# Optimization experiments

Hardware: AMD Instinct MI355X
Metric: run time of the kernel (lower is better)

Reference implementation:

```python
import jax, jax.numpy as jnp
import numpy as np

B, C, H, W = 2, 64, 256, 256
DW = 128          # c * DW_Expand
FFN = 128         # c * FFN_Expand
GRID = 8          # wH = wW modulation grid


def setup_inputs() -> dict:
    key = jax.random.key(0)
    ks = jax.random.split(key, 16)
    rn = lambda k, s, sc=1.0: jax.random.normal(k, s, jnp.float32) * sc
    return {
        "x": rn(ks[0], (B, C, H, W)),
        "w1": rn(ks[1], (DW, C), (2.0 / C) ** 0.5),
        "b1": jnp.zeros((DW,), jnp.float32),
        "w2": rn(ks[2], (DW, 3, 3), (2.0 / 9.0) ** 0.5),
        "b2": jnp.zeros((DW,), jnp.float32),
        "w3": rn(ks[3], (C, DW // 2), (2.0 / (DW // 2)) ** 0.5),
        "b3": jnp.zeros((C,), jnp.float32),
        "sca_w": rn(ks[4], (DW // 2, DW // 2), (1.0 / (DW // 2)) ** 0.5),
        "sca_b": jnp.zeros((DW // 2,), jnp.float32),
        "w4": rn(ks[5], (FFN, C), (2.0 / C) ** 0.5),
        "b4": jnp.zeros((FFN,), jnp.float32),
        "w5": rn(ks[6], (C, FFN // 2), (2.0 / (FFN // 2)) ** 0.5),
        "b5": jnp.zeros((C,), jnp.float32),
        "n1_w": jnp.ones((C,), jnp.float32),
        "n1_b": jnp.zeros((C,), jnp.float32),
        "n2_w": jnp.ones((C,), jnp.float32),
        "n2_b": jnp.zeros((C,), jnp.float32),
        "beta": rn(ks[7], (C,), 0.1),
        "gamma": rn(ks[8], (C,), 0.1),
        "mod1": rn(ks[9], (B, DW, C, GRID, GRID)),
        "mod2": rn(ks[10], (B, DW, GRID, GRID)),
        "mod3": rn(ks[11], (B, C, DW // 2, GRID, GRID)),
        "mod4": rn(ks[12], (B, FFN, C, GRID, GRID)),
        "mod5": rn(ks[13], (B, C, FFN // 2, GRID, GRID)),
    }


def layernorm2d(x, w, b, eps=1e-6):
    # channel-wise LayerNorm per pixel (NAFNet LayerNorm2d)
    mu = jnp.mean(x, axis=1, keepdims=True)
    var = jnp.mean((x - mu) ** 2, axis=1, keepdims=True)
    return (x - mu) / jnp.sqrt(var + eps) * w[None, :, None, None] + b[None, :, None, None]


def conv1x1_modulated(x, wb, bb, mod):
    # wb: [Co,Ci], mod: [B,Co,Ci,wH,wW]; per-patch 1x1 conv with normalized dynamic weights
    w = wb[None, :, :, None, None] * mod                      # [B,Co,Ci,wH,wW]
    w = w / jnp.sqrt(jnp.sum(w * w, axis=2, keepdims=True))   # normalize over Ci (kh*kw==1)
    b_, ci, h, wd = x.shape
    wh, ww = mod.shape[-2:]
    ph, pw = h // wh, wd // ww
    xp = x.reshape(b_, ci, wh, ph, ww, pw)                    # split into patches
    y = jnp.einsum('bocuv,bcupvq->boupvq', w, xp)             # per-patch matmul
    return y.reshape(b_, wb.shape[0], h, wd) + bb[None, :, None, None]


def conv3x3_dw_modulated(x, wb, bb, mod):
    # wb: [C,3,3], mod: [B,C,wH,wW]; per-patch depthwise 3x3, padding 1 across whole image
    w = wb[None, :, :, :, None, None] * mod[:, :, None, None, :, :]  # [B,C,3,3,wH,wW]
    w = w / jnp.sqrt(jnp.sum(w * w, axis=(2, 3), keepdims=True))     # normalize over (ci=1, kh*kw)
    b_, c, h, wd = x.shape
    wh, ww = mod.shape[-2:]
    ph, pw = h // wh, wd // ww
    xpad = jnp.pad(x, ((0, 0), (0, 0), (1, 1), (1, 1)))
    out = jnp.zeros_like(x)
    for dh in range(3):
        for dw_ in range(3):
            xs = xpad[:, :, dh:dh + h, dw_:dw_ + wd].reshape(b_, c, wh, ph, ww, pw)
            wk = w[:, :, dh, dw_, :, :]                        # [B,C,wH,wW]
            out = out + (wk[:, :, :, None, :, None] * xs).reshape(b_, c, h, wd)
    return out + bb[None, :, None, None]


def simple_gate(x):
    a, g = jnp.split(x, 2, axis=1)
    return a * g


def reference(x, w1, b1, w2, b2, w3, b3, sca_w, sca_b, w4, b4, w5, b5,
              n1_w, n1_b, n2_w, n2_b, beta, gamma, mod1, mod2, mod3, mod4, mod5):
    y = layernorm2d(x, n1_w, n1_b)
    y = conv1x1_modulated(y, w1, b1, mod1)
    y = conv3x3_dw_modulated(y, w2, b2, mod2)
    y = simple_gate(y)
    s = jnp.mean(y, axis=(2, 3), keepdims=True)               # SCA: global pool + 1x1
    s = jnp.einsum('oc,bcij->boij', sca_w, s) + sca_b[None, :, None, None]
    y = y * s
    y = conv1x1_modulated(y, w3, b3, mod3)
    y1 = x + y * beta[None, :, None, None]
    z = conv1x1_modulated(layernorm2d(y1, n2_w, n2_b), w4, b4, mod4)
    z = simple_gate(z)
    z = conv1x1_modulated(z, w5, b5, mod5)
    return y1 + z * gamma[None, :, None, None]
```

## Files before the change

### kernel.cpp

```cpp
#include <hip/hip_runtime.h>
#include <hip/hip_bf16.h>


typedef __bf16 bf16x8 __attribute__((ext_vector_type(8)));
typedef float f32x4 __attribute__((ext_vector_type(4)));
typedef unsigned short u16x8 __attribute__((ext_vector_type(8)));

__device__ __forceinline__ float b2f(unsigned short u) {
    union { unsigned int i; float f; } x; x.i = ((unsigned int)u) << 16; return x.f;
}
__device__ __forceinline__ unsigned short f2b(float f) {
    union { float f; unsigned int i; } x; x.f = f;
    unsigned int i = x.i;
    return (unsigned short)((i + 0x7FFFu + ((i >> 16) & 1u)) >> 16);
}
__device__ __forceinline__ unsigned int pk2(float a, float b) {
    __hip_bfloat162 h = __float22bfloat162_rn(float2{a, b});
    union { __hip_bfloat162 h; unsigned int u; } cv; cv.h = h; return cv.u;
}

__global__ __launch_bounds__(256) void prep_k(
    const float* __restrict__ w1, const float* __restrict__ mod1,
    const float* __restrict__ w3, const float* __restrict__ mod3,
    const float* __restrict__ beta,
    const float* __restrict__ w4, const float* __restrict__ mod4,
    const float* __restrict__ w5, const float* __restrict__ mod5,
    const float* __restrict__ gam,
    unsigned short* __restrict__ pw1, unsigned short* __restrict__ pw3,
    unsigned short* __restrict__ pw4, unsigned short* __restrict__ pw5,
    float* __restrict__ s0)
{
    const int tid = threadIdx.x;
    int blk = blockIdx.x;
    if (blk == 0 && tid < 128) s0[tid] = 0.f;
    const float* w; const float* mod; const float* rows = nullptr;
    unsigned short* out; int NOUT; int rem;
    if (blk < 256)      { w = w1; mod = mod1; out = pw1; NOUT = 128; rem = blk; }
    else if (blk < 384) { w = w3; mod = mod3; out = pw3; NOUT = 64;  rem = blk - 256; rows = beta; }
    else if (blk < 640) { w = w4; mod = mod4; out = pw4; NOUT = 128; rem = blk - 384; }
    else                { w = w5; mod = mod5; out = pw5; NOUT = 64;  rem = blk - 640; rows = gam; }
    const int b = rem / NOUT, o = rem % NOUT;

    __shared__ float mlds[64 * 68];
    __shared__ float wlsh[64];
    __shared__ float red[4 * 64];
    __shared__ float rs[64];

    const float* mbase = mod + ((size_t)(b * NOUT + o) * 64) * 64;
#pragma unroll
    for (int k = 0; k < 4; ++k) {
        int l = tid + k * 256;
        float4 vv = ((const float4*)mbase)[l];
        int c = l >> 4, q = l & 15;
        *(float4*)&mlds[c * 68 + q * 4] = vv;
    }
    if (tid < 64) wlsh[tid] = w[o * 64 + tid];
    __syncthreads();

    {
        int uv = tid & 63, part = tid >> 6;
        float ss = 0.f;
#pragma unroll
        for (int j = 0; j < 16; ++j) {
            int c = part * 16 + j;
            float t = wlsh[c] * mlds[c * 68 + uv];
            ss += t * t;
        }
        red[part * 64 + uv] = ss;
    }
    __syncthreads();
    if (tid < 64) {
        float tot = red[tid] + red[64 + tid] + red[128 + tid] + red[192 + tid];
        rs[tid] = rsqrtf(fmaxf(tot, 1e-30f)) * (rows ? rows[o] : 1.f);
    }
    __syncthreads();

    {
        int uvw = tid >> 2, cp = tid & 3;
        float r = rs[uvw];
        size_t obase = ((size_t)(b * 64 + uvw) * NOUT + o) * 64;
#pragma unroll
        for (int g = 0; g < 2; ++g) {
            u16x8 pk;
#pragma unroll
            for (int e = 0; e < 8; ++e) {
                int c = cp * 16 + g * 8 + e;
                pk[e] = f2b(wlsh[c] * mlds[c * 68 + uvw] * r);
            }
            *(u16x8*)&out[obase + cp * 16 + g * 8] = pk;
        }
    }
}

__global__ __launch_bounds__(256, 2) void head_k(
    const float* __restrict__ x, unsigned short* __restrict__ t1,
    const unsigned short* __restrict__ pw1, const float* __restrict__ b1,
    const float* __restrict__ n1w, const float* __restrict__ n1b, int bbase)
{
    const int tid   = threadIdx.x;
    const int uv    = blockIdx.x;
    const int chunk = blockIdx.y;
    const int z     = blockIdx.z;
    const int bfull = z + bbase;
    const int u = uv >> 3, v = uv & 7;
    const int h_base = u * 32 + chunk * 4;
    const int w_base = v * 32;

    __shared__ __align__(16) unsigned short stage[128 * 72];

    const int wave = tid >> 6;
    const int lane = tid & 63;
    const int q = lane >> 4;
    const int r = lane & 15;
    const int nfi[2] = {2 * wave, 2 * wave + 1};

    const unsigned short* pwt = pw1 + ((size_t)(bfull * 64 + uv) * 128) * 64;
    bf16x8 bfr[2][2];
#pragma unroll
    for (int f = 0; f < 2; ++f)
#pragma unroll
        for (int ks = 0; ks < 2; ++ks)
            bfr[f][ks] = *(const bf16x8*)&pwt[(16 * nfi[f] + r) * 64 + ks * 32 + q * 8];
    float bsc[2] = {b1[16 * nfi[0] + r], b1[16 * nfi[1] + r]};

    const int cg = tid & 7;
    const int qd = tid >> 3;
    const int c0 = cg * 8;
    const int pixg = (h_base + (qd >> 3)) * 256 + w_base + (qd & 7) * 4;
    float v2[8][4];
#pragma unroll
    for (int k = 0; k < 8; ++k) {
        float4 t = *(const float4*)&x[((z * 64 + c0 + k) << 16) + pixg];
        v2[k][0] = t.x; v2[k][1] = t.y; v2[k][2] = t.z; v2[k][3] = t.w;
    }
    float lw[8], lb[8];
    *(float4*)&lw[0] = *(const float4*)&n1w[c0];
    *(float4*)&lw[4] = *(const float4*)&n1w[c0 + 4];
    *(float4*)&lb[0] = *(const float4*)&n1b[c0];
    *(float4*)&lb[4] = *(const float4*)&n1b[c0 + 4];
#pragma unroll
    for (int e = 0; e < 4; ++e) {
        float s1 = 0.f, s2 = 0.f;
#pragma unroll
        for (int k = 0; k < 8; ++k) { s1 += v2[k][e]; s2 += v2[k][e] * v2[k][e]; }
#pragma unroll
        for (int m = 1; m < 8; m <<= 1) { s1 += __shfl_xor(s1, m); s2 += __shfl_xor(s2, m); }
        float mu = s1 * (1.f / 64.f);
        float var = s2 * (1.f / 64.f) - mu * mu;
        float rstd = rsqrtf(fmaxf(var, 0.f) + 1e-6f);
        float o8[8];
#pragma unroll
        for (int k = 0; k < 8; ++k) o8[k] = (v2[k][e] - mu) * rstd * lw[k] + lb[k];
        uint4 pk;
        pk.x = pk2(o8[0], o8[1]); pk.y = pk2(o8[2], o8[3]);
        pk.z = pk2(o8[4], o8[5]); pk.w = pk2(o8[6], o8[7]);
        *(uint4*)&stage[(qd * 4 + e) * 72 + c0] = pk;
    }

    __syncthreads();

    f32x4 acc[8][2];
#pragma unroll
    for (int mi = 0; mi < 8; ++mi) { acc[mi][0] = (f32x4){0,0,0,0}; acc[mi][1] = (f32x4){0,0,0,0}; }
#pragma unroll
    for (int mi = 0; mi < 8; ++mi) {
        bf16x8 a0 = *(const bf16x8*)&stage[(16 * mi + r) * 72 + q * 8];
        bf16x8 a1 = *(const bf16x8*)&stage[(16 * mi + r) * 72 + 32 + q * 8];
#pragma unroll
        for (int f = 0; f < 2; ++f) {
            acc[mi][f] = __builtin_amdgcn_mfma_f32_16x16x32_bf16(a0, bfr[f][0], acc[mi][f], 0, 0, 0);
            acc[mi][f] = __builtin_amdgcn_mfma_f32_16x16x32_bf16(a1, bfr[f][1], acc[mi][f], 0, 0, 0);
        }
    }

#pragma unroll
    for (int mi = 0; mi < 8; ++mi) {
        int lp0 = 16 * mi + 4 * q;
        int pix = (h_base + (lp0 >> 5)) * 256 + w_base + (lp0 & 31);
#pragma unroll
        for (int f = 0; f < 2; ++f) {
            int o = 16 * nfi[f] + r;
            float bs = bsc[f];
            *(uint2*)&t1[((z * 128 + o) << 16) + pix] =
                make_uint2(pk2(acc[mi][f][0] + bs, acc[mi][f][1] + bs),
                           pk2(acc[mi][f][2] + bs, acc[mi][f][3] + bs));
        }
    }
}

__global__ __launch_bounds__(256, 2) void tail_k(
    const unsigned short* __restrict__ t3, const float* __restrict__ x,
    float* __restrict__ outp,
    const unsigned short* __restrict__ pw3, const float* __restrict__ b3,
    const float* __restrict__ beta,
    const unsigned short* __restrict__ pw4, const float* __restrict__ b4,
    const float* __restrict__ n2w, const float* __restrict__ n2b,
    const unsigned short* __restrict__ pw5, const float* __restrict__ b5,
    const float* __restrict__ gam,
    const float* __restrict__ scaw, const float* __restrict__ scab,
    const float* __restrict__ s0, int bbase)
{
    const int tid   = threadIdx.x;
    const int uv    = blockIdx.x;
    const int chunk = blockIdx.y;
    const int z     = blockIdx.z;
    const int bfull = z + bbase;
    const int u = uv >> 3, v = uv & 7;
    const int h_base = u * 32 + chunk * 4;
    const int w_base = v * 32;

    __shared__ __align__(16) unsigned short stage[128 * 72];
    __shared__ float sfin_l[64];

    const int wave = tid >> 6;
    const int lane = tid & 63;
    const int q = lane >> 4;
    const int r = lane & 15;
    const int oo = 16 * wave + r;

    if (tid < 64) {
        const float* srow = scaw + tid * 64;
        const float* s0b  = s0 + bfull * 64;
        float acc = 0.f;
#pragma unroll
        for (int c4 = 0; c4 < 16; ++c4) {
            float4 wv = *(const float4*)&srow[c4 * 4];
            float4 s4 = *(const float4*)&s0b[c4 * 4];
            acc += wv.x * s4.x + wv.y * s4.y + wv.z * s4.z + wv.w * s4.w;
        }
        sfin_l[tid] = acc * (1.f / 65536.f) + scab[tid];
    }

    const unsigned short* p3 = pw3 + (size_t)(bfull * 64 + uv) * 64 * 64;
    const unsigned short* p4 = pw4 + (size_t)(bfull * 64 + uv) * 128 * 64;
    const unsigned short* p5 = pw5 + (size_t)(bfull * 64 + uv) * 64 * 64;
    bf16x8 w3f[2], w5f[2], w4f[2][2];
    const int nfi4[2] = {wave, wave + 4};
#pragma unroll
    for (int ks = 0; ks < 2; ++ks) {
        w3f[ks] = *(const bf16x8*)&p3[(oo) * 64 + ks * 32 + q * 8];
        w5f[ks] = *(const bf16x8*)&p5[(oo) * 64 + ks * 32 + q * 8];
#pragma unroll
        for (int f = 0; f < 2; ++f)
            w4f[f][ks] = *(const bf16x8*)&p4[(16 * nfi4[f] + r) * 64 + ks * 32 + q * 8];
    }
    const float sb3 = b3[oo] * beta[oo];
    const float ba4 = b4[oo], bg4 = b4[oo + 64];
    const float sb5 = b5[oo] * gam[oo];

    __syncthreads();

    const int cg = tid & 7;
    const int qd = tid >> 3;
    const int c0 = cg * 8;
    const int pixg = (h_base + (qd >> 3)) * 256 + w_base + (qd & 7) * 4;
    {
        float sv[8];
        *(float4*)&sv[0] = *(const float4*)&sfin_l[c0];
        *(float4*)&sv[4] = *(const float4*)&sfin_l[c0 + 4];
        float v2[8][4];
#pragma unroll
        for (int k = 0; k < 8; ++k) {
            ushort4 t = *(const ushort4*)&t3[((z * 64 + c0 + k) << 16) + pixg];
            v2[k][0] = b2f(t.x) * sv[k]; v2[k][1] = b2f(t.y) * sv[k];
            v2[k][2] = b2f(t.z) * sv[k]; v2[k][3] = b2f(t.w) * sv[k];
        }
#pragma unroll
        for (int e = 0; e < 4; ++e) {
            uint4 pk;
            pk.x = pk2(v2[0][e], v2[1][e]); pk.y = pk2(v2[2][e], v2[3][e]);
            pk.z = pk2(v2[4][e], v2[5][e]); pk.w = pk2(v2[6][e], v2[7][e]);
            *(uint4*)&stage[(qd * 4 + e) * 72 + c0] = pk;
        }
    }
    __syncthreads();

    f32x4 acc3[8];
#pragma unroll
    for (int mi = 0; mi < 8; ++mi) acc3[mi] = (f32x4){0, 0, 0, 0};
#pragma unroll
    for (int mi = 0; mi < 8; ++mi) {
        bf16x8 a0 = *(const bf16x8*)&stage[(16 * mi + r) * 72 + q * 8];
        bf16x8 a1 = *(const bf16x8*)&stage[(16 * mi + r) * 72 + 32 + q * 8];
        acc3[mi] = __builtin_amdgcn_mfma_f32_16x16x32_bf16(a0, w3f[0], acc3[mi], 0, 0, 0);
        acc3[mi] = __builtin_amdgcn_mfma_f32_16x16x32_bf16(a1, w3f[1], acc3[mi], 0, 0, 0);
    }
    __syncthreads();

    float y1v[8][4];
#pragma unroll
    for (int mi = 0; mi < 8; ++mi) {
        int lp0 = 16 * mi + 4 * q;
        int pix = (h_base + (lp0 >> 5)) * 256 + w_base + (lp0 & 31);
        float4 xr = *(const float4*)&x[((z * 64 + oo) << 16) + pix];
        y1v[mi][0] = acc3[mi][0] + sb3 + xr.x;
        y1v[mi][1] = acc3[mi][1] + sb3 + xr.y;
        y1v[mi][2] = acc3[mi][2] + sb3 + xr.z;
        y1v[mi][3] = acc3[mi][3] + sb3 + xr.w;
    }
#pragma unroll
    for (int mi = 0; mi < 8; ++mi)
#pragma unroll
        for (int e = 0; e < 4; ++e)
            stage[(16 * mi + 4 * q + e) * 72 + oo] = f2b(y1v[mi][e]);
    __syncthreads();

    {
        float lw[8], lb[8];
        *(float4*)&lw[0] = *(const float4*)&n2w[c0];
        *(float4*)&lw[4] = *(const float4*)&n2w[c0 + 4];
        *(float4*)&lb[0] = *(const float4*)&n2b[c0];
        *(float4*)&lb[4] = *(const float4*)&n2b[c0 + 4];
#pragma unroll
        for (int e = 0; e < 4; ++e) {
            int px = qd * 4 + e;
            uint4 raw = *(const uint4*)&stage[px * 72 + c0];
            unsigned short* rp = (unsigned short*)&raw;
            float vv[8];
            float s1 = 0.f, s2 = 0.f;
#pragma unroll
            for (int k = 0; k < 8; ++k) { vv[k] = b2f(rp[k]); s1 += vv[k]; s2 += vv[k] * vv[k]; }
#pragma unroll
            for (int m = 1; m < 8; m <<= 1) { s1 += __shfl_xor(s1, m); s2 += __shfl_xor(s2, m); }
            float mu = s1 * (1.f / 64.f);
            float var = s2 * (1.f / 64.f) - mu * mu;
            float rstd = rsqrtf(fmaxf(var, 0.f) + 1e-6f);
            float o8[8];
#pragma unroll
            for (int k = 0; k < 8; ++k) o8[k] = (vv[k] - mu) * rstd * lw[k] + lb[k];
            uint4 pk;
            pk.x = pk2(o8[0], o8[1]); pk.y = pk2(o8[2], o8[3]);
            pk.z = pk2(o8[4], o8[5]); pk.w = pk2(o8[6], o8[7]);
            *(uint4*)&stage[px * 72 + c0] = pk;
        }
    }
    __syncthreads();

    f32x4 acc4[8][2];
#pragma unroll
    for (int mi = 0; mi < 8; ++mi) { acc4[mi][0] = (f32x4){0,0,0,0}; acc4[mi][1] = (f32x4){0,0,0,0}; }
#pragma unroll
    for (int mi = 0; mi < 8; ++mi) {
        bf16x8 a0 = *(const bf16x8*)&stage[(16 * mi + r) * 72 + q * 8];
        bf16x8 a1 = *(const bf16x8*)&stage[(16 * mi + r) * 72 + 32 + q * 8];
#pragma unroll
        for (int f = 0; f < 2; ++f) {
            acc4[mi][f] = __builtin_amdgcn_mfma_f32_16x16x32_bf16(a0, w4f[f][0], acc4[mi][f], 0, 0, 0);
            acc4[mi][f] = __builtin_amdgcn_mfma_f32_16x16x32_bf16(a1, w4f[f][1], acc4[mi][f], 0, 0, 0);
        }
    }
    __syncthreads();
#pragma unroll
    for (int mi = 0; mi < 8; ++mi)
#pragma unroll
        for (int e = 0; e < 4; ++e) {
            float zv = (acc4[mi][0][e] + ba4) * (acc4[mi][1][e] + bg4);
            stage[(16 * mi + 4 * q + e) * 72 + oo] = f2b(zv);
        }
    __syncthreads();

    f32x4 acc5[8];
#pragma unroll
    for (int mi = 0; mi < 8; ++mi) acc5[mi] = (f32x4){0, 0, 0, 0};
#pragma unroll
    for (int mi = 0; mi < 8; ++mi) {
        bf16x8 a0 = *(const bf16x8*)&stage[(16 * mi + r) * 72 + q * 8];
        bf16x8 a1 = *(const bf16x8*)&stage[(16 * mi + r) * 72 + 32 + q * 8];
        acc5[mi] = __builtin_amdgcn_mfma_f32_16x16x32_bf16(a0, w5f[0], acc5[mi], 0, 0, 0);
        acc5[mi] = __builtin_amdgcn_mfma_f32_16x16x32_bf16(a1, w5f[1], acc5[mi], 0, 0, 0);
    }
#pragma unroll
    for (int mi = 0; mi < 8; ++mi) {
        int lp0 = 16 * mi + 4 * q;
        int pix = (h_base + (lp0 >> 5)) * 256 + w_base + (lp0 & 31);
        *(float4*)&outp[((z * 64 + oo) << 16) + pix] =
            make_float4(y1v[mi][0] + acc5[mi][0] + sb5,
                        y1v[mi][1] + acc5[mi][1] + sb5,
                        y1v[mi][2] + acc5[mi][2] + sb5,
                        y1v[mi][3] + acc5[mi][3] + sb5);
    }
}

__global__ __launch_bounds__(256, 4) void dw_k(
    const unsigned short* __restrict__ t1,
    unsigned short* __restrict__ t3,
    const float* __restrict__ w2,
    const float* __restrict__ b2,
    const float* __restrict__ mod2,
    float* __restrict__ s0,
    int bbase)
{
    const int tid  = threadIdx.x;
    const int oc   = blockIdx.x;
    const int band = blockIdx.y;
    const int z    = blockIdx.z;
    const int bfull = z + bbase;
    const int u = band >> 2;

    __shared__ float wl[2][8][9];
    __shared__ float wred[4];

    if (tid < 16) {
        int halfc = tid >> 3, vv = tid & 7;
        const float* wrow = w2 + (oc + halfc * 64) * 9;
        float wloc[9], ssum = 0.f;
#pragma unroll
        for (int k = 0; k < 9; ++k) { wloc[k] = wrow[k]; ssum += wloc[k] * wloc[k]; }
        float m = mod2[(bfull * 128 + oc + halfc * 64) * 64 + u * 8 + vv];
        float rn = m * rsqrtf(fmaxf(m * m * ssum, 1e-30f));
#pragma unroll
        for (int k = 0; k < 9; ++k) wl[halfc][vv][k] = wloc[k] * rn;
    }
    __syncthreads();

    const int strip = tid & 31;
    const int row   = band * 8 + (tid >> 5);
    const int v     = strip >> 2;

    float wa[9], wg[9];
#pragma unroll
    for (int k = 0; k < 9; ++k) { wa[k] = wl[0][v][k]; wg[k] = wl[1][v][k]; }
    const float ba = b2[oc], bg = b2[oc + 64];

    const unsigned short* pa = t1 + (((size_t)z * 128 + oc) << 16);
    const unsigned short* pg = pa + ((size_t)64 << 16);

    float fa[3][8], fg[3][8], la[3], ra[3], lg[3], rg[3];
#pragma unroll
    for (int dr = 0; dr < 3; ++dr) {
        int rr = row - 1 + dr;
        if (rr >= 0 && rr < 256) {
            u16x8 va = *(const u16x8*)&pa[rr * 256 + strip * 8];
            u16x8 vg = *(const u16x8*)&pg[rr * 256 + strip * 8];
#pragma unroll
            for (int e = 0; e < 8; ++e) { fa[dr][e] = b2f(va[e]); fg[dr][e] = b2f(vg[e]); }
        } else {
#pragma unroll
            for (int e = 0; e < 8; ++e) { fa[dr][e] = 0.f; fg[dr][e] = 0.f; }
        }
        float t;
        t = __shfl_up(fa[dr][7], 1);   la[dr] = (strip == 0)  ? 0.f : t;
        t = __shfl_up(fg[dr][7], 1);   lg[dr] = (strip == 0)  ? 0.f : t;
        t = __shfl_down(fa[dr][0], 1); ra[dr] = (strip == 31) ? 0.f : t;
        t = __shfl_down(fg[dr][0], 1); rg[dr] = (strip == 31) ? 0.f : t;
    }

    float psum = 0.f;
    u16x8 pk;
#pragma unroll
    for (int j = 0; j < 8; ++j) {
        float a = 0.f, g = 0.f;
#pragma unroll
        for (int dr = 0; dr < 3; ++dr) {
            float m1a = (j == 0) ? la[dr] : fa[dr][j - 1];
            float p1a = (j == 7) ? ra[dr] : fa[dr][j + 1];
            float m1g = (j == 0) ? lg[dr] : fg[dr][j - 1];
            float p1g = (j == 7) ? rg[dr] : fg[dr][j + 1];
            a += wa[dr * 3] * m1a + wa[dr * 3 + 1] * fa[dr][j] + wa[dr * 3 + 2] * p1a;
            g += wg[dr * 3] * m1g + wg[dr * 3 + 1] * fg[dr][j] + wg[dr * 3 + 2] * p1g;
        }
        float val = (a + ba) * (g + bg);
        psum += val;
        pk[j] = f2b(val);
    }
    *(u16x8*)&t3[(((size_t)z * 64 + oc) << 16) + row * 256 + strip * 8] = pk;

    for (int off = 32; off > 0; off >>= 1) psum += __shfl_down(psum, off, 64);
    if ((tid & 63) == 0) wred[tid >> 6] = psum;
    __syncthreads();
    if (tid == 0)
        atomicAdd(&s0[bfull * 64 + oc], wred[0] + wred[1] + wred[2] + wred[3]);
}

extern "C" void kernel_launch(void* const* d_in, const int* in_sizes, int n_in,
                              void* d_out, int out_size, void* d_ws, size_t ws_size,
                              hipStream_t stream) {
    (void)in_sizes; (void)n_in; (void)out_size;
    const float* x    = (const float*)d_in[0];
    const float* w1   = (const float*)d_in[1];
    const float* b1   = (const float*)d_in[2];
    const float* w2   = (const float*)d_in[3];
    const float* b2   = (const float*)d_in[4];
    const float* w3   = (const float*)d_in[5];
    const float* b3   = (const float*)d_in[6];
    const float* scaw = (const float*)d_in[7];
    const float* scab = (const float*)d_in[8];
    const float* w4   = (const float*)d_in[9];
    const float* b4   = (const float*)d_in[10];
    const float* w5   = (const float*)d_in[11];
    const float* b5   = (const float*)d_in[12];
    const float* n1w  = (const float*)d_in[13];
    const float* n1b  = (const float*)d_in[14];
    const float* n2w  = (const float*)d_in[15];
    const float* n2b  = (const float*)d_in[16];
    const float* beta = (const float*)d_in[17];
    const float* gam  = (const float*)d_in[18];
    const float* mod1 = (const float*)d_in[19];
    const float* mod2 = (const float*)d_in[20];
    const float* mod3 = (const float*)d_in[21];
    const float* mod4 = (const float*)d_in[22];
    const float* mod5 = (const float*)d_in[23];

    char* ws = (char*)d_ws;
    float* outf = (float*)d_out;

    const size_t IMGel = (size_t)64 * 65536;
    const size_t T1B   = (size_t)128 * 65536 * 2;
    const size_t T3B   = (size_t)64 * 65536 * 2;
    const size_t PW1B = 2097152, PW3B = 1048576, PW4B = 2097152, PW5B = 1048576;
    const size_t TBLB = PW1B + PW3B + PW4B + PW5B;

    const size_t needA = 2 * (T1B + T3B) + 4096 + TBLB;
    const bool planA = ws_size >= needA;
    const size_t NBT = planA ? 2 : 1;

    unsigned short* t1 = (unsigned short*)ws;
    unsigned short* t3 = (unsigned short*)(ws + NBT * T1B);
    char* statb = ws + NBT * (T1B + T3B);
    float* s0   = (float*)statb;
    unsigned short* pw1 = (unsigned short*)(statb + 4096);
    unsigned short* pw3 = (unsigned short*)(statb + 4096 + PW1B);
    unsigned short* pw4 = (unsigned short*)(statb + 4096 + PW1B + PW3B);
    unsigned short* pw5 = (unsigned short*)(statb + 4096 + PW1B + PW3B + PW4B);

    dim3 blk(256);

    prep_k<<<768, blk, 0, stream>>>(w1, mod1, w3, mod3, beta, w4, mod4,
                                    w5, mod5, gam, pw1, pw3, pw4, pw5, s0);

    if (planA) {
        dim3 gconv(64, 8, 2), gdw(64, 32, 2);
        head_k<<<gconv, blk, 0, stream>>>(x, t1, pw1, b1, n1w, n1b, 0);
        dw_k<<<gdw, blk, 0, stream>>>(t1, t3, w2, b2, mod2, s0, 0);
        tail_k<<<gconv, blk, 0, stream>>>(t3, x, outf, pw3, b3, beta,
                                          pw4, b4, n2w, n2b, pw5, b5, gam,
                                          scaw, scab, s0, 0);
    } else {
        for (int bb = 0; bb < 2; ++bb) {
            const float* x_b   = x    + (size_t)bb * IMGel;
            float*       out_b = outf + (size_t)bb * IMGel;
            dim3 gconv(64, 8, 1), gdw(64, 32, 1);
            head_k<<<gconv, blk, 0, stream>>>(x_b, t1, pw1, b1, n1w, n1b, bb);
            dw_k<<<gdw, blk, 0, stream>>>(t1, t3, w2, b2, mod2, s0, bb);
            tail_k<<<gconv, blk, 0, stream>>>(t3, x_b, out_b, pw3, b3, beta,
                                              pw4, b4, n2w, n2b, pw5, b5, gam,
                                              scaw, scab, s0, bb);
        }
    }
}
```

Before: 202.3 us.

## Raise occupancy bounds, prefetch residual, nontemporal output stores, per-thread dw weights

Raises the launch-bounds occupancy hints for head_k to 4 and tail_k to 3 blocks per CU. tail_k now loads the residual x values at kernel entry so their latency overlaps the earlier phases, and it writes the output with nontemporal stores. dw_k drops the shared-memory weight setup and its barrier, and each thread instead computes its own normalized 3x3 weights. The higher occupancy targets can force register spills, and the early x prefetch keeps 32 extra live registers across the kernel.

```diff
diff --git a/kernel.cpp b/kernel.cpp
--- a/kernel.cpp
+++ b/kernel.cpp
@@ -92,7 +92,7 @@
     }
 }
 
-__global__ __launch_bounds__(256, 2) void head_k(
+__global__ __launch_bounds__(256, 4) void head_k(
     const float* __restrict__ x, unsigned short* __restrict__ t1,
     const unsigned short* __restrict__ pw1, const float* __restrict__ b1,
     const float* __restrict__ n1w, const float* __restrict__ n1b, int bbase)
@@ -188,7 +188,7 @@
     }
 }
 
-__global__ __launch_bounds__(256, 2) void tail_k(
+__global__ __launch_bounds__(256, 3) void tail_k(
     const unsigned short* __restrict__ t3, const float* __restrict__ x,
     float* __restrict__ outp,
     const unsigned short* __restrict__ pw3, const float* __restrict__ b3,
@@ -218,6 +218,14 @@
     const int r = lane & 15;
     const int oo = 16 * wave + r;
 
+    float4 xr8[8];
+#pragma unroll
+    for (int mi = 0; mi < 8; ++mi) {
+        int lp0 = 16 * mi + 4 * q;
+        int pix = (h_base + (lp0 >> 5)) * 256 + w_base + (lp0 & 31);
+        xr8[mi] = *(const float4*)&x[((z * 64 + oo) << 16) + pix];
+    }
+
     if (tid < 64) {
         const float* srow = scaw + tid * 64;
         const float* s0b  = s0 + bfull * 64;
@@ -290,13 +298,10 @@
     float y1v[8][4];
 #pragma unroll
     for (int mi = 0; mi < 8; ++mi) {
-        int lp0 = 16 * mi + 4 * q;
-        int pix = (h_base + (lp0 >> 5)) * 256 + w_base + (lp0 & 31);
-        float4 xr = *(const float4*)&x[((z * 64 + oo) << 16) + pix];
-        y1v[mi][0] = acc3[mi][0] + sb3 + xr.x;
-        y1v[mi][1] = acc3[mi][1] + sb3 + xr.y;
-        y1v[mi][2] = acc3[mi][2] + sb3 + xr.z;
-        y1v[mi][3] = acc3[mi][3] + sb3 + xr.w;
+        y1v[mi][0] = acc3[mi][0] + sb3 + xr8[mi].x;
+        y1v[mi][1] = acc3[mi][1] + sb3 + xr8[mi].y;
+        y1v[mi][2] = acc3[mi][2] + sb3 + xr8[mi].z;
+        y1v[mi][3] = acc3[mi][3] + sb3 + xr8[mi].w;
     }
 #pragma unroll
     for (int mi = 0; mi < 8; ++mi)
@@ -373,11 +378,11 @@
     for (int mi = 0; mi < 8; ++mi) {
         int lp0 = 16 * mi + 4 * q;
         int pix = (h_base + (lp0 >> 5)) * 256 + w_base + (lp0 & 31);
-        *(float4*)&outp[((z * 64 + oo) << 16) + pix] =
-            make_float4(y1v[mi][0] + acc5[mi][0] + sb5,
-                        y1v[mi][1] + acc5[mi][1] + sb5,
-                        y1v[mi][2] + acc5[mi][2] + sb5,
-                        y1v[mi][3] + acc5[mi][3] + sb5);
+        f32x4 ov = {y1v[mi][0] + acc5[mi][0] + sb5,
+                    y1v[mi][1] + acc5[mi][1] + sb5,
+                    y1v[mi][2] + acc5[mi][2] + sb5,
+                    y1v[mi][3] + acc5[mi][3] + sb5};
+        __builtin_nontemporal_store(ov, (f32x4*)&outp[((z * 64 + oo) << 16) + pix]);
     }
 }
 
@@ -397,29 +402,29 @@
     const int bfull = z + bbase;
     const int u = band >> 2;
 
-    __shared__ float wl[2][8][9];
     __shared__ float wred[4];
-
-    if (tid < 16) {
-        int halfc = tid >> 3, vv = tid & 7;
-        const float* wrow = w2 + (oc + halfc * 64) * 9;
-        float wloc[9], ssum = 0.f;
-#pragma unroll
-        for (int k = 0; k < 9; ++k) { wloc[k] = wrow[k]; ssum += wloc[k] * wloc[k]; }
-        float m = mod2[(bfull * 128 + oc + halfc * 64) * 64 + u * 8 + vv];
-        float rn = m * rsqrtf(fmaxf(m * m * ssum, 1e-30f));
-#pragma unroll
-        for (int k = 0; k < 9; ++k) wl[halfc][vv][k] = wloc[k] * rn;
-    }
-    __syncthreads();
 
     const int strip = tid & 31;
     const int row   = band * 8 + (tid >> 5);
     const int v     = strip >> 2;
 
     float wa[9], wg[9];
-#pragma unroll
-    for (int k = 0; k < 9; ++k) { wa[k] = wl[0][v][k]; wg[k] = wl[1][v][k]; }
+    {
+        const float* wra = w2 + oc * 9;
+        const float* wrg = w2 + (oc + 64) * 9;
+        float ssa = 0.f, ssg = 0.f;
+#pragma unroll
+        for (int k = 0; k < 9; ++k) {
+            wa[k] = wra[k]; ssa += wa[k] * wa[k];
+            wg[k] = wrg[k]; ssg += wg[k] * wg[k];
+        }
+        float ma = mod2[(bfull * 128 + oc) * 64 + u * 8 + v];
+        float mg = mod2[(bfull * 128 + oc + 64) * 64 + u * 8 + v];
+        float rna = ma * rsqrtf(fmaxf(ma * ma * ssa, 1e-30f));
+        float rng = mg * rsqrtf(fmaxf(mg * mg * ssg, 1e-30f));
+#pragma unroll
+        for (int k = 0; k < 9; ++k) { wa[k] *= rna; wg[k] *= rng; }
+    }
     const float ba = b2[oc], bg = b2[oc + 64];
 
     const unsigned short* pa = t1 + (((size_t)z * 128 + oc) << 16);
```

New measurement: 200.2 us. Within noise of the previous version (-1.0%).
